# Kernel optimization log

Measured on AMD Instinct MI355X. Metric: run time of the kernel, lower is better.

Reference implementation:

```python
import jax, jax.numpy as jnp
import numpy as np

DIM = 768
NUM_HEADS = 16
HEAD_DIM = DIM // NUM_HEADS
SCALE = HEAD_DIM ** -0.5


def setup_inputs() -> dict:
    key = jax.random.key(0)
    ks = jax.random.split(key, 9)
    B, S = 4, 2048
    init = 1.0 / np.sqrt(DIM)
    x = jax.random.normal(ks[0], (B, S, DIM), dtype=jnp.float32)
    Wq = jax.random.uniform(ks[1], (DIM, DIM), jnp.float32, -init, init)
    bq = jax.random.uniform(ks[2], (DIM,), jnp.float32, -init, init)
    Wk = jax.random.uniform(ks[3], (DIM, DIM), jnp.float32, -init, init)
    bk = jax.random.uniform(ks[4], (DIM,), jnp.float32, -init, init)
    Wv = jax.random.uniform(ks[5], (DIM, DIM), jnp.float32, -init, init)
    bv = jax.random.uniform(ks[6], (DIM,), jnp.float32, -init, init)
    Wo = jax.random.uniform(ks[7], (DIM, DIM), jnp.float32, -init, init)
    bo = jax.random.uniform(ks[8], (DIM,), jnp.float32, -init, init)
    return {"x": x, "Wq": Wq, "bq": bq, "Wk": Wk, "bk": bk,
            "Wv": Wv, "bv": bv, "Wo": Wo, "bo": bo}


def reference(x, Wq, bq, Wk, bk, Wv, bv, Wo, bo):
    B, S, D = x.shape
    H, Hd = NUM_HEADS, HEAD_DIM
    # Linear layers (torch Linear: y = x @ W^T + b); split heads -> [B,H,S,Hd]
    q = (x @ Wq.T + bq).reshape(B, S, H, Hd).transpose(0, 2, 1, 3)
    k = (x @ Wk.T + bk).reshape(B, S, H, Hd).transpose(0, 2, 1, 3)
    v = (x @ Wv.T + bv).reshape(B, S, H, Hd).transpose(0, 2, 1, 3)
    scores = jnp.einsum('bhqd,bhkd->bhqk', q, k) * SCALE  # [B,H,S,S]
    attn = jax.nn.softmax(scores, axis=-1)
    # dropout is identity in eval mode
    out = jnp.einsum('bhqk,bhkd->bhqd', attn, v)
    out = out.transpose(0, 2, 1, 3).reshape(B, S, D)
    return out @ Wo.T + bo
```

## Files before the change

### kernel.cpp

```cpp
#include <hip/hip_runtime.h>

typedef __bf16 bf16_t;
typedef bf16_t bf16x8 __attribute__((ext_vector_type(8)));
typedef _Float16 f16_t;
typedef __fp16 hf16x2 __attribute__((ext_vector_type(2)));
typedef f16_t f16x8 __attribute__((ext_vector_type(8)));
typedef float floatx4 __attribute__((ext_vector_type(4)));
typedef float floatx16 __attribute__((ext_vector_type(16)));

#define S_LEN 2048
#define DIM 768
#define NH 16
#define HD 48
#define HDP 64
#define BHEADS 64
#define ATT_SCALE 0.14433756729740643f
#define W_ELEMS (DIM * DIM)

typedef unsigned short u16;
typedef unsigned int u32;

__device__ __forceinline__ u16 f2b(float f) {
  union { float f; u32 i; } z; z.f = f;
  u32 i = z.i;
  return (u16)((i + 0x7fffu + ((i >> 16) & 1u)) >> 16);
}
__device__ __forceinline__ u32 pack2(float a, float b) {
  return (u32)f2b(a) | ((u32)f2b(b) << 16);
}
__device__ __forceinline__ u32 pkrtz2(float a, float b) {
  union { hf16x2 h; u32 u; } z;
  z.h = __builtin_amdgcn_cvt_pkrtz(a, b);
  return z.u;
}
__device__ __forceinline__ void pl32swap(u32& a, u32& b) {
  asm("v_permlane32_swap_b32 %0, %1" : "+v"(a), "+v"(b));
}
__device__ __forceinline__ void gld_lds16(const void* g, void* l) {
  __builtin_amdgcn_global_load_lds(
      (const __attribute__((address_space(1))) u32*)g,
      (__attribute__((address_space(3))) u32*)l, 16, 0, 0);
}

__global__ __launch_bounds__(256) void cvt_all(
    const float* __restrict__ x,
    const float* __restrict__ w0, const float* __restrict__ w1,
    const float* __restrict__ w2, const float* __restrict__ w3,
    u16* __restrict__ x_dst, u16* __restrict__ w_dst)
{
  const int blk = blockIdx.x;
  const float* src;
  u16* dst;
  int idx;
  if (blk < 3072) {
    src = x; dst = x_dst; idx = blk * 256 + threadIdx.x;
  } else {
    int wb = blk - 3072;
    int j = wb / 288;
    src = (j == 0) ? w0 : (j == 1) ? w1 : (j == 2) ? w2 : w3;
    dst = w_dst + (size_t)j * W_ELEMS;
    idx = (wb - j * 288) * 256 + threadIdx.x;
  }
  const float4* s = (const float4*)src;
  float4 a = s[idx * 2], b = s[idx * 2 + 1];
  *(uint4*)&dst[(size_t)idx * 8] =
      make_uint4(pack2(a.x, a.y), pack2(a.z, a.w), pack2(b.x, b.y), pack2(b.z, b.w));
}


__global__ __launch_bounds__(256) void gemm_qkv(
    const u16* __restrict__ A, const u16* __restrict__ Wbase,
    const float* __restrict__ bq, const float* __restrict__ bk,
    const float* __restrict__ bv,
    u16* __restrict__ q_out, u16* __restrict__ k_out, u16* __restrict__ v_out)
{
  __shared__ __attribute__((aligned(16))) u16 smem[8704];
  u16* As = smem;
  u16* Bs = smem + 4096;

  const int tid = threadIdx.x;
  const int w = tid >> 6, lane = tid & 63, lo = lane & 15, quad = lane >> 4;
  const int wr = w >> 1, wc = w & 1;
  const int bm = blockIdx.x & 63, bn = blockIdx.x >> 6;
  const int mat = bn / 6;
  const int n0 = (bn - mat * 6) * 128;
  const int m0 = bm * 128;
  const u16* W = Wbase + (size_t)mat * W_ELEMS;
  const float* bias = mat == 0 ? bq : (mat == 1 ? bk : bv);
  const float scale = mat == 0 ? ATT_SCALE : 1.0f;

  size_t aoff[2], boff[2];
#pragma unroll
  for (int it = 0; it < 2; ++it) {
    int c = tid + it * 256, r = c >> 2, ccl = c & 3;
    int ccg = ccl ^ ((r >> 1) & 3);
    aoff[it] = (size_t)(m0 + r) * DIM + ccg * 8;
    boff[it] = (size_t)(n0 + r) * DIM + ccg * 8;
  }

  floatx4 acc[4][4];
#pragma unroll
  for (int mi = 0; mi < 4; mi++)
#pragma unroll
    for (int ni = 0; ni < 4; ni++) acc[mi][ni] = (floatx4){0.f, 0.f, 0.f, 0.f};

  for (int k0 = 0; k0 < DIM; k0 += 32) {
    __syncthreads();
#pragma unroll
    for (int it = 0; it < 2; ++it) {
      gld_lds16(&A[aoff[it] + k0], &As[(it * 256 + w * 64) * 8]);
      gld_lds16(&W[boff[it] + k0], &Bs[(it * 256 + w * 64) * 8]);
    }
    __syncthreads();

    bf16x8 af[4], bfr[4];
#pragma unroll
    for (int mi = 0; mi < 4; mi++) {
      int row = wr * 64 + mi * 16 + lo;
      int s = quad ^ ((row >> 1) & 3);
      af[mi] = *(const bf16x8*)&As[row * 32 + s * 8];
    }
#pragma unroll
    for (int ni = 0; ni < 4; ni++) {
      int row = wc * 64 + ni * 16 + lo;
      int s = quad ^ ((row >> 1) & 3);
      bfr[ni] = *(const bf16x8*)&Bs[row * 32 + s * 8];
    }
#pragma unroll
    for (int mi = 0; mi < 4; mi++)
#pragma unroll
      for (int ni = 0; ni < 4; ni++)
        acc[mi][ni] = __builtin_amdgcn_mfma_f32_16x16x32_bf16(af[mi], bfr[ni], acc[mi][ni], 0, 0, 0);
  }

  if (mat == 2) {
    u16 (*T)[136] = (u16(*)[136])smem;
    const int b = m0 >> 11, s0 = m0 & 2047;
#pragma unroll
    for (int half = 0; half < 2; ++half) {
      __syncthreads();
      if (wc == half) {
#pragma unroll
        for (int mi = 0; mi < 4; mi++)
#pragma unroll
          for (int ni = 0; ni < 4; ni++) {
            int colL = ni * 16 + lo;
            float bb = bias[n0 + half * 64 + colL];
            float v0 = acc[mi][ni][0] + bb, v1 = acc[mi][ni][1] + bb;
            float v2 = acc[mi][ni][2] + bb, v3 = acc[mi][ni][3] + bb;
            *(uint2*)&T[colL][wr * 64 + mi * 16 + quad * 4] =
                make_uint2(pkrtz2(v0, v1), pkrtz2(v2, v3));
          }
      }
      __syncthreads();
#pragma unroll
      for (int it = 0; it < 4; ++it) {
        int ch = tid + it * 256;
        int col = ch >> 4, sc = ch & 15;
        int gcol = n0 + half * 64 + col;
        int h = gcol / HD, d = gcol - h * HD;
        size_t dst = ((size_t)(b * NH + h) * HDP + d) * S_LEN + s0 + sc * 8;
        *(uint4*)&v_out[dst] = *(const uint4*)&T[col][sc * 8];
      }
    }
    return;
  }

  u16* out = mat == 0 ? q_out : k_out;
#pragma unroll
  for (int mi = 0; mi < 4; mi++)
#pragma unroll
    for (int ni = 0; ni < 4; ni++)
#pragma unroll
      for (int r = 0; r < 4; r++) {
        int row = m0 + wr * 64 + mi * 16 + quad * 4 + r;
        int col = n0 + wc * 64 + ni * 16 + lo;
        float v = (acc[mi][ni][r] + bias[col]) * scale;
        int b = row >> 11, s = row & 2047;
        int h = col / HD, d = col - h * HD;
        out[((size_t)((b * NH + h) * S_LEN + s)) * HDP + d] = f2b(v);
      }
}

__global__ __launch_bounds__(256) void gemm_wo(
    const u16* __restrict__ A, const u16* __restrict__ W,
    const float* __restrict__ bias, float* __restrict__ out)
{
  __shared__ __attribute__((aligned(16))) u16 smem[6144];
  u16* As = smem;
  u16* Bs = smem + 4096;

  const int tid = threadIdx.x;
  const int w = tid >> 6, lane = tid & 63, lo = lane & 15, quad = lane >> 4;
  const int bm = blockIdx.x & 63, bn = blockIdx.x >> 6;
  const int m0 = bm * 128, n0 = bn * 64;

  int ar[2], accg[2];
#pragma unroll
  for (int it = 0; it < 2; ++it) {
    int c = tid + it * 256, r = c >> 2, ccl = c & 3;
    ar[it] = m0 + r;
    accg[it] = (ccl ^ ((r >> 1) & 3)) * 8;
  }
  size_t boff;
  {
    int r = tid >> 2, ccl = tid & 3;
    boff = (size_t)(n0 + r) * DIM + (ccl ^ ((r >> 1) & 3)) * 8;
  }

  floatx4 acc[2][4];
#pragma unroll
  for (int mi = 0; mi < 2; mi++)
#pragma unroll
    for (int ni = 0; ni < 4; ni++) acc[mi][ni] = (floatx4){0.f, 0.f, 0.f, 0.f};

  for (int k0 = 0; k0 < DIM; k0 += 32) {
    __syncthreads();
#pragma unroll
    for (int it = 0; it < 2; ++it) {
      int row = ar[it], c8 = k0 + accg[it];
      int h = c8 / HD, d = c8 - h * HD;
      int b = row >> 11, s = row & 2047;
      gld_lds16(&A[((size_t)((b * NH + h) * S_LEN + s)) * HD + d],
                &As[(it * 256 + w * 64) * 8]);
    }
    gld_lds16(&W[boff + k0], &Bs[(w * 64) * 8]);
    __syncthreads();

    bf16x8 af[2], bfr[4];
#pragma unroll
    for (int mi = 0; mi < 2; mi++) {
      int row = w * 32 + mi * 16 + lo;
      int s = quad ^ ((row >> 1) & 3);
      af[mi] = *(const bf16x8*)&As[row * 32 + s * 8];
    }
#pragma unroll
    for (int ni = 0; ni < 4; ni++) {
      int row = ni * 16 + lo;
      int s = quad ^ ((row >> 1) & 3);
      bfr[ni] = *(const bf16x8*)&Bs[row * 32 + s * 8];
    }
#pragma unroll
    for (int mi = 0; mi < 2; mi++)
#pragma unroll
      for (int ni = 0; ni < 4; ni++)
        acc[mi][ni] = __builtin_amdgcn_mfma_f32_16x16x32_bf16(af[mi], bfr[ni], acc[mi][ni], 0, 0, 0);
  }

#pragma unroll
  for (int mi = 0; mi < 2; mi++)
#pragma unroll
    for (int ni = 0; ni < 4; ni++)
#pragma unroll
      for (int r = 0; r < 4; r++) {
        int row = m0 + w * 32 + mi * 16 + quad * 4 + r;
        int col = n0 + ni * 16 + lo;
        out[(size_t)row * DIM + col] = acc[mi][ni][r] + bias[col];
      }
}

#define STG_LOAD(k0n) do {                                                     \
  _Pragma("unroll")                                                            \
  for (int it = 0; it < 3; ++it) {                                             \
    int c = tid + it * 256;                                                    \
    if (c < 384) {                                                             \
      int r = c / 6, cc = c - r * 6;                                           \
      stg[it] = *(const uint4*)&K[base + (size_t)((k0n) + r) * HDP + cc * 8];  \
    } else {                                                                   \
      int c2 = c - 384, r = c2 >> 3, cc = c2 & 7;                              \
      stg[it] = *(const uint4*)&V[base + (size_t)r * S_LEN + (k0n) + cc * 8];  \
    }                                                                          \
  }                                                                            \
} while (0)

#define STG_WRITE(bufi) do {                                                   \
  _Pragma("unroll")                                                            \
  for (int it = 0; it < 3; ++it) {                                             \
    int c = tid + it * 256;                                                    \
    if (c < 384) {                                                             \
      int r = c / 6, cc = c - r * 6;                                           \
      *(uint4*)&Ks[bufi][r][cc * 8] = stg[it];                                 \
    } else {                                                                   \
      int c2 = c - 384, r = c2 >> 3, cc = c2 & 7;                              \
      *(uint4*)&Vt[bufi][r][cc * 8] = stg[it];                                 \
    }                                                                          \
  }                                                                            \
} while (0)

__global__ __launch_bounds__(256, 2) void attn_kernel(
    const u16* __restrict__ Q, const u16* __restrict__ K,
    const u16* __restrict__ V, u16* __restrict__ O)
{
  __shared__ __attribute__((aligned(16))) u16 Ks[2][64][56];
  __shared__ __attribute__((aligned(16))) u16 Vt[2][64][72];

  const int tid = threadIdx.x;
  const int w = tid >> 6, lane = tid & 63, l31 = lane & 31, hi = lane >> 5;
  const int flat = blockIdx.x;
  const int xcd = flat & 7, sub = flat >> 3;
  const int bh = xcd * 8 + (sub >> 3);
  const int q0 = (sub & 7) * 256;
  const size_t base = (size_t)bh * S_LEN * HDP;

  bf16x8 qf[2][3];
#pragma unroll
  for (int t = 0; t < 2; t++)
#pragma unroll
    for (int ks = 0; ks < 3; ks++)
      qf[t][ks] = *(const bf16x8*)
          &Q[base + (size_t)(q0 + w * 64 + t * 32 + l31) * HDP + ks * 16 + hi * 8];

  floatx16 oacc[2][2];
#pragma unroll
  for (int t = 0; t < 2; t++)
#pragma unroll
    for (int nd = 0; nd < 2; nd++)
#pragma unroll
      for (int r = 0; r < 16; r++) oacc[t][nd][r] = 0.f;

  float l_lane[2] = {0.f, 0.f};

  uint4 stg[3];
  STG_LOAD(0);
  STG_WRITE(0);

  for (int ti = 0; ti < 32; ++ti) {
    const int cur = ti & 1;
    if (ti < 31) STG_LOAD((ti + 1) * 64);
    __syncthreads();

    bf16x8 ak[2][3];
#pragma unroll
    for (int na = 0; na < 2; na++)
#pragma unroll
      for (int ks = 0; ks < 3; ks++)
        ak[na][ks] = *(const bf16x8*)&Ks[cur][na * 32 + l31][ks * 16 + hi * 8];

    u32 pk[2][2][8];
#pragma unroll
    for (int t = 0; t < 2; t++) {
      floatx16 s0, s1;
#pragma unroll
      for (int r = 0; r < 16; r++) { s0[r] = 0.f; s1[r] = 0.f; }
#pragma unroll
      for (int ks = 0; ks < 3; ks++) {
        s0 = __builtin_amdgcn_mfma_f32_32x32x16_bf16(ak[0][ks], qf[t][ks], s0, 0, 0, 0);
        s1 = __builtin_amdgcn_mfma_f32_32x32x16_bf16(ak[1][ks], qf[t][ks], s1, 0, 0, 0);
      }
#pragma unroll
      for (int m = 0; m < 8; m++) {
        float a0 = __expf(s0[2 * m]), a1 = __expf(s0[2 * m + 1]);
        float b0 = __expf(s1[2 * m]), b1 = __expf(s1[2 * m + 1]);
        l_lane[t] += (a0 + a1) + (b0 + b1);
        pk[t][0][m] = pkrtz2(a0, a1);
        pk[t][1][m] = pkrtz2(b0, b1);
      }
    }

#pragma unroll
    for (int kt = 0; kt < 4; kt++) {
      f16x8 bv0 = *(const f16x8*)&Vt[cur][l31][kt * 16 + hi * 8];
      f16x8 bv1 = *(const f16x8*)&Vt[cur][32 + l31][kt * 16 + hi * 8];
      const int na = kt >> 1, k4 = (kt & 1) * 4;
#pragma unroll
      for (int t = 0; t < 2; t++) {
        u32 w0 = pk[t][na][k4 + 0], w2 = pk[t][na][k4 + 2];
        u32 w1 = pk[t][na][k4 + 1], w3 = pk[t][na][k4 + 3];
        pl32swap(w0, w2);
        pl32swap(w1, w3);
        union { u32 u[4]; f16x8 f; } af;
        af.u[0] = w0; af.u[1] = w1; af.u[2] = w2; af.u[3] = w3;
        oacc[t][0] = __builtin_amdgcn_mfma_f32_32x32x16_f16(af.f, bv0, oacc[t][0], 0, 0, 0);
        oacc[t][1] = __builtin_amdgcn_mfma_f32_32x32x16_f16(af.f, bv1, oacc[t][1], 0, 0, 0);
      }
    }

    if (ti < 31) STG_WRITE(cur ^ 1);
  }

  const size_t obase = (size_t)bh * S_LEN * HD;
  float lt_full[2];
#pragma unroll
  for (int t = 0; t < 2; t++)
    lt_full[t] = l_lane[t] + __shfl_xor(l_lane[t], 32);
#pragma unroll
  for (int t = 0; t < 2; t++) {
#pragma unroll
    for (int r = 0; r < 16; r++) {
      int q_local = (r & 3) + 8 * (r >> 2) + 4 * hi;
      float l_r = __shfl(lt_full[t], q_local);
      float inv = 1.f / l_r;
      int q = q0 + w * 64 + t * 32 + q_local;
      u16* orow = O + obase + (size_t)q * HD;
      orow[l31] = f2b(oacc[t][0][r] * inv);
      if (l31 < 16) orow[32 + l31] = f2b(oacc[t][1][r] * inv);
    }
  }
}

extern "C" void kernel_launch(void* const* d_in, const int* in_sizes, int n_in,
                              void* d_out, int out_size, void* d_ws, size_t ws_size,
                              hipStream_t stream)
{
  const float* x  = (const float*)d_in[0];
  const float* Wq = (const float*)d_in[1];
  const float* bq = (const float*)d_in[2];
  const float* Wk = (const float*)d_in[3];
  const float* bk = (const float*)d_in[4];
  const float* Wv = (const float*)d_in[5];
  const float* bv = (const float*)d_in[6];
  const float* Wo = (const float*)d_in[7];
  const float* bo = (const float*)d_in[8];

  u16* ws   = (u16*)d_ws;
  const size_t qkv_elems = (size_t)BHEADS * S_LEN * HDP;
  u16* q_ws = ws;
  u16* k_ws = q_ws + qkv_elems;
  u16* v_ws = k_ws + qkv_elems;
  u16* x_bf = v_ws + qkv_elems;
  u16* a_ws = x_bf;
  u16* w_bf = x_bf + (size_t)8192 * DIM;
  u16* wo_bf = w_bf + (size_t)3 * W_ELEMS;

  cvt_all<<<dim3(4224), dim3(256), 0, stream>>>(x, Wq, Wk, Wv, Wo, x_bf, w_bf);
  gemm_qkv<<<dim3(1152), dim3(256), 0, stream>>>(x_bf, w_bf, bq, bk, bv,
                                                 q_ws, k_ws, v_ws);
  attn_kernel<<<dim3(512), dim3(256), 0, stream>>>(q_ws, k_ws, v_ws, a_ws);
  gemm_wo<<<dim3(768), dim3(256), 0, stream>>>(a_ws, wo_bf, bo, (float*)d_out);
}
```

Before: 257.6 us.

## Split attention KV range across two blocks and add combine kernel

```diff
diff --git a/kernel.cpp b/kernel.cpp
--- a/kernel.cpp
+++ b/kernel.cpp
@@ -287,9 +287,11 @@
   }                                                                            \
 } while (0)
 
+template<int NSPLIT>
 __global__ __launch_bounds__(256, 2) void attn_kernel(
     const u16* __restrict__ Q, const u16* __restrict__ K,
-    const u16* __restrict__ V, u16* __restrict__ O)
+    const u16* __restrict__ V, u16* __restrict__ O,
+    float* __restrict__ Op, float* __restrict__ Lp)
 {
   __shared__ __attribute__((aligned(16))) u16 Ks[2][64][56];
   __shared__ __attribute__((aligned(16))) u16 Vt[2][64][72];
@@ -298,8 +300,18 @@
   const int w = tid >> 6, lane = tid & 63, l31 = lane & 31, hi = lane >> 5;
   const int flat = blockIdx.x;
   const int xcd = flat & 7, sub = flat >> 3;
-  const int bh = xcd * 8 + (sub >> 3);
-  const int q0 = (sub & 7) * 256;
+  int bh, q0, sp;
+  if constexpr (NSPLIT == 2) {
+    bh = xcd * 8 + (sub >> 4);
+    q0 = ((sub >> 1) & 7) * 256;
+    sp = sub & 1;
+  } else {
+    bh = xcd * 8 + (sub >> 3);
+    q0 = (sub & 7) * 256;
+    sp = 0;
+  }
+  const int NT = (NSPLIT == 2) ? 16 : 32;
+  const int kbase = sp * NT * 64;
   const size_t base = (size_t)bh * S_LEN * HDP;
 
   bf16x8 qf[2][3];
@@ -321,12 +333,12 @@
   float l_lane[2] = {0.f, 0.f};
 
   uint4 stg[3];
-  STG_LOAD(0);
+  STG_LOAD(kbase);
   STG_WRITE(0);
 
-  for (int ti = 0; ti < 32; ++ti) {
+  for (int ti = 0; ti < NT; ++ti) {
     const int cur = ti & 1;
-    if (ti < 31) STG_LOAD((ti + 1) * 64);
+    if (ti < NT - 1) STG_LOAD(kbase + (ti + 1) * 64);
     __syncthreads();
 
     bf16x8 ak[2][3];
@@ -375,26 +387,66 @@
       }
     }
 
-    if (ti < 31) STG_WRITE(cur ^ 1);
-  }
-
-  const size_t obase = (size_t)bh * S_LEN * HD;
+    if (ti < NT - 1) STG_WRITE(cur ^ 1);
+  }
+
   float lt_full[2];
 #pragma unroll
   for (int t = 0; t < 2; t++)
     lt_full[t] = l_lane[t] + __shfl_xor(l_lane[t], 32);
-#pragma unroll
-  for (int t = 0; t < 2; t++) {
-#pragma unroll
-    for (int r = 0; r < 16; r++) {
-      int q_local = (r & 3) + 8 * (r >> 2) + 4 * hi;
-      float l_r = __shfl(lt_full[t], q_local);
-      float inv = 1.f / l_r;
-      int q = q0 + w * 64 + t * 32 + q_local;
-      u16* orow = O + obase + (size_t)q * HD;
-      orow[l31] = f2b(oacc[t][0][r] * inv);
-      if (l31 < 16) orow[32 + l31] = f2b(oacc[t][1][r] * inv);
-    }
+
+  if constexpr (NSPLIT == 2) {
+    const size_t qbase = (size_t)bh * S_LEN + q0;
+    if (hi == 0) {
+#pragma unroll
+      for (int t = 0; t < 2; t++)
+        Lp[(size_t)sp * BHEADS * S_LEN + qbase + w * 64 + t * 32 + l31] = lt_full[t];
+    }
+    float* Ob = Op + (size_t)sp * BHEADS * S_LEN * HD;
+#pragma unroll
+    for (int t = 0; t < 2; t++)
+#pragma unroll
+      for (int r = 0; r < 16; r++) {
+        int q_local = (r & 3) + 8 * (r >> 2) + 4 * hi;
+        size_t ro = (qbase + w * 64 + t * 32 + q_local) * HD;
+        Ob[ro + l31] = oacc[t][0][r];
+        if (l31 < 16) Ob[ro + 32 + l31] = oacc[t][1][r];
+      }
+  } else {
+    const size_t obase = (size_t)bh * S_LEN * HD;
+#pragma unroll
+    for (int t = 0; t < 2; t++) {
+#pragma unroll
+      for (int r = 0; r < 16; r++) {
+        int q_local = (r & 3) + 8 * (r >> 2) + 4 * hi;
+        float l_r = __shfl(lt_full[t], q_local);
+        float inv = 1.f / l_r;
+        int q = q0 + w * 64 + t * 32 + q_local;
+        u16* orow = O + obase + (size_t)q * HD;
+        orow[l31] = f2b(oacc[t][0][r] * inv);
+        if (l31 < 16) orow[32 + l31] = f2b(oacc[t][1][r] * inv);
+      }
+    }
+  }
+}
+
+__global__ __launch_bounds__(256) void attn_combine(
+    const float* __restrict__ Op, const float* __restrict__ Lp,
+    u16* __restrict__ out)
+{
+  const size_t OFF = (size_t)BHEADS * S_LEN * HD;
+  const size_t LOFF = (size_t)BHEADS * S_LEN;
+  const int t0 = blockIdx.x * 3072 + threadIdx.x;
+#pragma unroll
+  for (int j = 0; j < 12; ++j) {
+    int f = t0 + j * 256;
+    int row = f / 12;
+    float4 a = ((const float4*)Op)[f];
+    float4 b = ((const float4*)(Op + OFF))[f];
+    float inv = 1.f / (Lp[row] + Lp[LOFF + row]);
+    float v0 = (a.x + b.x) * inv, v1 = (a.y + b.y) * inv;
+    float v2 = (a.z + b.z) * inv, v3 = (a.w + b.w) * inv;
+    *(uint2*)&out[(size_t)f * 4] = make_uint2(pack2(v0, v1), pack2(v2, v3));
   }
 }
 
@@ -422,9 +474,23 @@
   u16* w_bf = x_bf + (size_t)8192 * DIM;
   u16* wo_bf = w_bf + (size_t)3 * W_ELEMS;
 
+  const size_t OFF = (size_t)BHEADS * S_LEN * HD;
+  float* Op = (float*)(w_bf + (size_t)4 * W_ELEMS);
+  float* Lp = Op + 2 * OFF;
+  const size_t needed_bytes =
+      (size_t)((u16*)Lp - ws) * 2 + 2 * BHEADS * S_LEN * 4;
+  const bool use_split = ws_size >= needed_bytes;
+
   cvt_all<<<dim3(4224), dim3(256), 0, stream>>>(x, Wq, Wk, Wv, Wo, x_bf, w_bf);
   gemm_qkv<<<dim3(1152), dim3(256), 0, stream>>>(x_bf, w_bf, bq, bk, bv,
                                                  q_ws, k_ws, v_ws);
-  attn_kernel<<<dim3(512), dim3(256), 0, stream>>>(q_ws, k_ws, v_ws, a_ws);
+  if (use_split) {
+    attn_kernel<2><<<dim3(1024), dim3(256), 0, stream>>>(
+        q_ws, k_ws, v_ws, a_ws, Op, Lp);
+    attn_combine<<<dim3(512), dim3(256), 0, stream>>>(Op, Lp, a_ws);
+  } else {
+    attn_kernel<1><<<dim3(512), dim3(256), 0, stream>>>(
+        q_ws, k_ws, v_ws, a_ws, Op, Lp);
+  }
   gemm_wo<<<dim3(768), dim3(256), 0, stream>>>(a_ws, wo_bf, bo, (float*)d_out);
 }
```

Result: slower. 272.9 us (+5.9%).
